# Kernel optimization log

Hardware: AMD Instinct MI355X
Metric: run time of the kernel (lower is better)

Reference implementation:

```python
import jax, jax.numpy as jnp
import numpy as np

MARGIN = 1.0
EPS = 1e-05
B = 8192
D = 128
NUM_CLASSES = 256


def setup_inputs() -> dict:
    key = jax.random.key(0)
    k1, k2 = jax.random.split(key)
    feature = jax.random.normal(k1, (B, D), dtype=jnp.float32)
    label = jax.random.randint(k2, (B,), 0, NUM_CLASSES, dtype=jnp.int32)
    return {"feature": feature, "label": label}


def reference(feature, label):
    # Pairwise Euclidean distance matrix: ||x_i||^2 + ||x_j||^2 - 2 x_i.x_j + eps, then sqrt
    sq = jnp.sum(feature * feature, axis=1, keepdims=True)  # [B, 1]
    dist = jnp.sqrt(jnp.maximum(sq + sq.T - 2.0 * (feature @ feature.T) + EPS, 0.0))  # [B, B]

    same = label[:, None] == label[None, :]  # [B, B] bool, includes self on diagonal
    inf = jnp.array(jnp.inf, dtype=dist.dtype)

    # Original sorts each row and takes same[1]: the SECOND smallest same-label distance
    # (the smallest is the anchor itself, distance sqrt(eps)).
    d_same = jnp.where(same, dist, inf)
    two_smallest = -jax.lax.top_k(-d_same, 2)[0]  # [B, 2], ascending smallest two
    pos = two_smallest[:, 1]  # nearest positive excluding self

    # diff.min(): hardest (closest) negative per row
    neg = jnp.min(jnp.where(same, inf, dist), axis=1)

    hinge = jnp.maximum(MARGIN + pos - neg, 0.0)
    return jnp.mean(hinge)
```

## Files before the change

kernel.cpp:

```cpp
#include <hip/hip_runtime.h>
#include <math.h>


#define BN 8192
#define MARGIN_F 1.0f
#define EPS_F 1e-5f

typedef __attribute__((ext_vector_type(8))) short short8;
typedef __attribute__((ext_vector_type(4))) float floatx4;

__device__ __forceinline__ unsigned short bf16_rne(float x, float& r) {
    unsigned u = __float_as_uint(x);
    u += 0x7FFF + ((u >> 16) & 1);
    unsigned short h = (unsigned short)(u >> 16);
    r = __uint_as_float(((unsigned)h) << 16);
    return h;
}

__global__ __launch_bounds__(256) void prep_kernel(const float* __restrict__ f,
                                                   const int* __restrict__ lbl,
                                                   short8* __restrict__ fbT,
                                                   float2* __restrict__ lsq,
                                                   float* __restrict__ g_acc,
                                                   unsigned* __restrict__ counter) {
    int gid = blockIdx.x * 256 + threadIdx.x;
    if (gid == 0) { *g_acc = 0.f; *counter = 0u; }
    int row = gid >> 3, part = gid & 7;
    const float4* f4 = (const float4*)f + (size_t)row * 32 + part * 4;
    float s = 0.f;
#pragma unroll
    for (int cc = 0; cc < 2; ++cc) {
        float4 v0 = f4[cc * 2], v1 = f4[cc * 2 + 1];
        float r0, r1, r2, r3, r4, r5, r6, r7;
        short8 o;
        o[0] = (short)bf16_rne(v0.x, r0);
        o[1] = (short)bf16_rne(v0.y, r1);
        o[2] = (short)bf16_rne(v0.z, r2);
        o[3] = (short)bf16_rne(v0.w, r3);
        o[4] = (short)bf16_rne(v1.x, r4);
        o[5] = (short)bf16_rne(v1.y, r5);
        o[6] = (short)bf16_rne(v1.z, r6);
        o[7] = (short)bf16_rne(v1.w, r7);
        fbT[(size_t)(part * 2 + cc) * BN + row] = o;
        s += r0 * r0 + r1 * r1 + r2 * r2 + r3 * r3 +
             r4 * r4 + r5 * r5 + r6 * r6 + r7 * r7;
    }
    s += __shfl_xor(s, 1, 8);
    s += __shfl_xor(s, 2, 8);
    s += __shfl_xor(s, 4, 8);
    if (part == 0) {
        float2 p;
        p.x = s;
        p.y = __int_as_float(lbl[row]);
        lsq[row] = p;
    }
}

template <bool DIAG>
__device__ __forceinline__ void jt_loop(const short8* __restrict__ bp,
                                        const float2* lsq_sh,
                                        const short8 a[2][4], const int li[2][4],
                                        float n1[2][4], float ss1[2][4],
                                        int c, int q, int i0, int jb) {
    for (int jt = 0; jt < 16; ++jt) {
        short8 b[4][2];
#pragma unroll
        for (int ks = 0; ks < 4; ++ks)
#pragma unroll
            for (int nf = 0; nf < 2; ++nf)
                b[ks][nf] = bp[(size_t)ks * 4 * BN + jt * 32 + nf * 16];

        int ljv[2]; float sjv[2];
#pragma unroll
        for (int nf = 0; nf < 2; ++nf) {
            float2 p = lsq_sh[jt * 32 + nf * 16 + c];
            sjv[nf] = p.x;
            ljv[nf] = __float_as_int(p.y);
        }

        int dd = DIAG ? ((i0 + q * 4) - (jb + jt * 32 + c)) : 0;

        floatx4 acc[2][2];
#pragma unroll
        for (int mf = 0; mf < 2; ++mf)
#pragma unroll
            for (int nf = 0; nf < 2; ++nf) acc[mf][nf] = (floatx4)0.f;

#pragma unroll
        for (int ks = 0; ks < 4; ++ks)
#pragma unroll
            for (int mf = 0; mf < 2; ++mf)
#pragma unroll
                for (int nf = 0; nf < 2; ++nf)
                    acc[mf][nf] = __builtin_amdgcn_mfma_f32_16x16x32_bf16(
                        a[mf][ks], b[ks][nf], acc[mf][nf], 0, 0, 0);

#pragma unroll
        for (int nf = 0; nf < 2; ++nf)
#pragma unroll
            for (int mf = 0; mf < 2; ++mf)
#pragma unroll
                for (int rg = 0; rg < 4; ++rg) {
                    float v = fmaf(-2.0f, acc[mf][nf][rg], sjv[nf]);
                    bool same = (li[mf][rg] == ljv[nf]);
                    float vd = same ? INFINITY : v;
                    n1[mf][rg] = fminf(n1[mf][rg], vd);
                    bool excl = same;
                    if (DIAG) excl = same && (dd != (nf * 16 - mf * 16 - rg));
                    float vs = excl ? v : INFINITY;
                    ss1[mf][rg] = fminf(ss1[mf][rg], vs);
                }
    }
}

__global__ __launch_bounds__(256, 4) void work_kernel(const short8* __restrict__ fbT,
                                                      const float2* __restrict__ lsq,
                                                      float* __restrict__ part_n1,
                                                      float* __restrict__ part_p1) {
    const int t = threadIdx.x;
    const int lane = t & 63;
    const int wv = t >> 6;
    const int q = lane >> 4, c = lane & 15;
    const int bid = blockIdx.x;

    __shared__ float2 lsq_sh[512];

    const int ib = bid & 63;
    const int g = bid >> 6;
    const int i0 = ib * 128 + wv * 32;
    const int jb = g * 512;
    const bool diag = ((ib >> 2) == g);

    lsq_sh[t] = lsq[jb + t];
    lsq_sh[t + 256] = lsq[jb + t + 256];

    short8 a[2][4];
#pragma unroll
    for (int mf = 0; mf < 2; ++mf) {
        int row = i0 + mf * 16 + c;
#pragma unroll
        for (int ks = 0; ks < 4; ++ks)
            a[mf][ks] = fbT[(size_t)(ks * 4 + q) * BN + row];
    }
    int li[2][4];
#pragma unroll
    for (int mf = 0; mf < 2; ++mf)
#pragma unroll
        for (int rg = 0; rg < 4; ++rg)
            li[mf][rg] = __float_as_int(lsq[i0 + mf * 16 + q * 4 + rg].y);

    float n1[2][4], ss1[2][4];
#pragma unroll
    for (int mf = 0; mf < 2; ++mf)
#pragma unroll
        for (int rg = 0; rg < 4; ++rg) {
            n1[mf][rg] = INFINITY;
            ss1[mf][rg] = INFINITY;
        }

    __syncthreads();

    const short8* bp = fbT + (size_t)q * BN + jb + c;
    if (diag)
        jt_loop<true>(bp, lsq_sh, a, li, n1, ss1, c, q, i0, jb);
    else
        jt_loop<false>(bp, lsq_sh, a, li, n1, ss1, c, q, i0, jb);

#pragma unroll
    for (int m = 1; m < 16; m <<= 1) {
#pragma unroll
        for (int mf = 0; mf < 2; ++mf)
#pragma unroll
            for (int rg = 0; rg < 4; ++rg) {
                n1[mf][rg] = fminf(n1[mf][rg], __shfl_xor(n1[mf][rg], m, 16));
                ss1[mf][rg] = fminf(ss1[mf][rg], __shfl_xor(ss1[mf][rg], m, 16));
            }
    }
    if (c == 0) {
#pragma unroll
        for (int mf = 0; mf < 2; ++mf)
#pragma unroll
            for (int rg = 0; rg < 4; ++rg) {
                int idx = g * BN + i0 + mf * 16 + q * 4 + rg;
                part_n1[idx] = n1[mf][rg];
                part_p1[idx] = ss1[mf][rg];
            }
    }
}

__global__ __launch_bounds__(128) void merge_kernel(const float* __restrict__ part_n1,
                                                    const float* __restrict__ part_p1,
                                                    const float2* __restrict__ lsq,
                                                    float* __restrict__ g_acc,
                                                    unsigned* __restrict__ counter,
                                                    float* __restrict__ out) {
    int r = blockIdx.x * 128 + threadIdx.x;
    float n = INFINITY, ss = INFINITY;
#pragma unroll
    for (int k = 0; k < 16; ++k) {
        n = fminf(n, part_n1[k * BN + r]);
        ss = fminf(ss, part_p1[k * BN + r]);
    }
    float si = lsq[r].x;
    float pos = sqrtf(fmaxf(si + ss + EPS_F, 0.f));
    float neg = sqrtf(fmaxf(si + n + EPS_F, 0.f));
    float h = fmaxf(MARGIN_F + pos - neg, 0.f);
    __shared__ float red[2];
#pragma unroll
    for (int m = 32; m >= 1; m >>= 1) h += __shfl_down(h, m, 64);
    if ((threadIdx.x & 63) == 0) red[threadIdx.x >> 6] = h;
    __syncthreads();
    if (threadIdx.x == 0) {
        atomicAdd(g_acc, red[0] + red[1]);
        __threadfence();
        unsigned old = atomicAdd(counter, 1u);
        if (old == 63u) {
            float tot = atomicAdd(g_acc, 0.0f);
            out[0] = tot / (float)BN;
        }
    }
}

extern "C" void kernel_launch(void* const* d_in, const int* in_sizes, int n_in,
                              void* d_out, int out_size, void* d_ws, size_t ws_size,
                              hipStream_t stream) {
    const float* f = (const float*)d_in[0];
    const int* lbl = (const int*)d_in[1];
    char* ws = (char*)d_ws;
    float2* lsq = (float2*)ws;
    short8* fbT = (short8*)(ws + 65536);
    float* part_n1 = (float*)(ws + 65536 + 2097152);
    float* part_p1 = (float*)(ws + 65536 + 2097152 + 524288);
    float* g_acc = (float*)(ws + 65536 + 2097152 + 1048576);
    unsigned* counter = (unsigned*)(g_acc + 1);
    float* out = (float*)d_out;

    prep_kernel<<<256, 256, 0, stream>>>(f, lbl, fbT, lsq, g_acc, counter);
    work_kernel<<<1024, 256, 0, stream>>>(fbT, lsq, part_n1, part_p1);
    merge_kernel<<<64, 128, 0, stream>>>(part_n1, part_p1, lsq, g_acc, counter, out);
}
```

Baseline: 85.97 us.

## Double-buffer shared B tiles in LDS via async global_load_lds

Instead of each wave loading its own copy of the B fragments from global memory every iteration, the block cooperatively stages each 32-column B tile into a double-buffered LDS array using global_load_lds. The next tile is prefetched while the current one is consumed. Waves then read their fragments from LDS. This cuts redundant global/L2 traffic by sharing one tile across the four waves and overlaps load latency with MFMA work. The cost is a block-wide barrier every iteration and 16KB of extra LDS per block.

```diff
diff --git a/kernel.cpp b/kernel.cpp
--- a/kernel.cpp
+++ b/kernel.cpp
@@ -56,19 +56,32 @@
     }
 }
 
+__device__ __forceinline__ void stage_tile(const short8* __restrict__ fbT,
+                                           short8* tile, int j0, int wv, int lane) {
+#pragma unroll
+    for (int it = 0; it < 2; ++it) {
+        int s = wv * 128 + it * 64;
+        int kc = (s >> 5) + (lane >> 5);
+        int col = lane & 31;
+        const short8* g = fbT + ((size_t)kc * BN + j0 + col);
+        __builtin_amdgcn_global_load_lds(
+            (const __attribute__((address_space(1))) void*)g,
+            (__attribute__((address_space(3))) void*)(tile + s),
+            16, 0, 0);
+    }
+}
+
 template <bool DIAG>
-__device__ __forceinline__ void jt_loop(const short8* __restrict__ bp,
+__device__ __forceinline__ void jt_loop(const short8* __restrict__ fbT,
+                                        short8 (*Bt)[512],
                                         const float2* lsq_sh,
                                         const short8 a[2][4], const int li[2][4],
                                         float n1[2][4], float ss1[2][4],
-                                        int c, int q, int i0, int jb) {
+                                        int wv, int lane, int c, int q,
+                                        int i0, int jb) {
     for (int jt = 0; jt < 16; ++jt) {
-        short8 b[4][2];
-#pragma unroll
-        for (int ks = 0; ks < 4; ++ks)
-#pragma unroll
-            for (int nf = 0; nf < 2; ++nf)
-                b[ks][nf] = bp[(size_t)ks * 4 * BN + jt * 32 + nf * 16];
+        const short8* cur = Bt[jt & 1];
+        if (jt < 15) stage_tile(fbT, Bt[1 - (jt & 1)], jb + (jt + 1) * 32, wv, lane);
 
         int ljv[2]; float sjv[2];
 #pragma unroll
@@ -79,6 +92,13 @@
         }
 
         int dd = DIAG ? ((i0 + q * 4) - (jb + jt * 32 + c)) : 0;
+
+        short8 b[4][2];
+#pragma unroll
+        for (int ks = 0; ks < 4; ++ks)
+#pragma unroll
+            for (int nf = 0; nf < 2; ++nf)
+                b[ks][nf] = cur[(ks * 4 + q) * 32 + nf * 16 + c];
 
         floatx4 acc[2][2];
 #pragma unroll
@@ -110,6 +130,7 @@
                     float vs = excl ? v : INFINITY;
                     ss1[mf][rg] = fminf(ss1[mf][rg], vs);
                 }
+        __syncthreads();
     }
 }
 
@@ -123,6 +144,7 @@
     const int q = lane >> 4, c = lane & 15;
     const int bid = blockIdx.x;
 
+    __shared__ short8 Bt[2][512];
     __shared__ float2 lsq_sh[512];
 
     const int ib = bid & 63;
@@ -131,6 +153,8 @@
     const int jb = g * 512;
     const bool diag = ((ib >> 2) == g);
 
+    stage_tile(fbT, Bt[0], jb, wv, lane);
+
     lsq_sh[t] = lsq[jb + t];
     lsq_sh[t + 256] = lsq[jb + t + 256];
 
@@ -160,11 +184,10 @@
 
     __syncthreads();
 
-    const short8* bp = fbT + (size_t)q * BN + jb + c;
     if (diag)
-        jt_loop<true>(bp, lsq_sh, a, li, n1, ss1, c, q, i0, jb);
+        jt_loop<true>(fbT, Bt, lsq_sh, a, li, n1, ss1, wv, lane, c, q, i0, jb);
     else
-        jt_loop<false>(bp, lsq_sh, a, li, n1, ss1, c, q, i0, jb);
+        jt_loop<false>(fbT, Bt, lsq_sh, a, li, n1, ss1, wv, lane, c, q, i0, jb);
 
 #pragma unroll
     for (int m = 1; m < 16; m <<= 1) {
```

After: 85.24 us. Within noise of the previous version (-0.9%).
